# Performance work log

Measured on AMD Instinct MI355X. Metric: run time of the kernel, lower is better.

## Reference

```python
import jax, jax.numpy as jnp
import numpy as np

N = 50000          # nodes
E = 800000         # edges (avg degree 16)
T = 4              # edge types (edge_attr_dim)
H = 8              # heads
C1 = 16            # state_dim (per-head channels, layer 1)
C2 = 8             # out_dim  (per-head channels, layer 2)
D = 128            # node_attr_dim
NEG = -1e9         # masked-attention logit
LRELU_SLOPE = 0.2  # PyG GATConv default negative_slope


def setup_inputs() -> dict:
    key = jax.random.key(0)
    ks = jax.random.split(key, 12)
    x = jax.random.normal(ks[0], (N, D), jnp.float32)
    edge_src = jax.random.randint(ks[1], (E,), 0, N, jnp.int32)
    edge_dst = jax.random.randint(ks[2], (E,), 0, N, jnp.int32)
    edge_type = jax.random.randint(ks[3], (E,), 0, T, jnp.int32)
    W1 = jax.random.normal(ks[4], (T, D, H * C1), jnp.float32) * (1.0 / np.sqrt(D))
    a1_src = jax.random.normal(ks[5], (T, H, C1), jnp.float32) * 0.1
    a1_dst = jax.random.normal(ks[6], (T, H, C1), jnp.float32) * 0.1
    b1 = jnp.zeros((T, H * C1), jnp.float32)
    W2 = jax.random.normal(ks[7], (T, H * C1, H * C2), jnp.float32) * (1.0 / np.sqrt(H * C1))
    a2_src = jax.random.normal(ks[8], (T, H, C2), jnp.float32) * 0.1
    a2_dst = jax.random.normal(ks[9], (T, H, C2), jnp.float32) * 0.1
    b2 = jnp.zeros((T, H * C2), jnp.float32)
    return dict(x=x, edge_src=edge_src, edge_dst=edge_dst, edge_type=edge_type,
                W1=W1, a1_src=a1_src, a1_dst=a1_dst, b1=b1,
                W2=W2, a2_src=a2_src, a2_dst=a2_dst, b2=b2)


def gat_conv(x_in, W, a_src, a_dst, b, src, dst, mask, n):
    """One PyG-style GATConv (concat heads, eval mode) on masked edge list."""
    heads, c = a_src.shape
    h = (x_in @ W).reshape(n, heads, c)                       # [N,H,C]
    s_src = jnp.sum(h * a_src, axis=-1)                        # [N,H]
    s_dst = jnp.sum(h * a_dst, axis=-1)                        # [N,H]
    e = jax.nn.leaky_relu(s_src[src] + s_dst[dst], LRELU_SLOPE)  # [Et,H]
    e = jnp.where(mask[:, None], e, NEG)
    m = jax.ops.segment_max(e, dst, num_segments=n)            # [N,H]
    p = jnp.exp(e - m[dst]) * mask[:, None].astype(e.dtype)    # unnorm softmax
    denom = jax.ops.segment_sum(p, dst, num_segments=n)        # [N,H]
    msg = p[:, :, None] * h[src]                               # [Et,H,C]
    agg = jax.ops.segment_sum(msg, dst, num_segments=n)        # [N,H,C]
    out = agg / denom[:, :, None]
    return out.reshape(n, heads * c) + b


def reference(x, edge_src, edge_dst, edge_type, W1, a1_src, a1_dst, b1,
              W2, a2_src, a2_dst, b2):
    n = x.shape[0]
    loops = jnp.arange(n, dtype=edge_src.dtype)
    src = jnp.concatenate([edge_src, loops])   # self-loops appended (PyG default)
    dst = jnp.concatenate([edge_dst, loops])
    ones = jnp.ones((n,), bool)
    outs = []
    for t in range(T):
        mask = jnp.concatenate([edge_type == t, ones])
        h1 = gat_conv(x, W1[t], a1_src[t], a1_dst[t], b1[t], src, dst, mask, n)
        h1 = jax.nn.relu(h1)
        h2 = gat_conv(h1, W2[t], a2_src[t], a2_dst[t], b2[t], src, dst, mask, n)
        outs.append(h2)
    return jnp.concatenate(outs, axis=1)       # [N, T*H*C2]
```

## Files before the change

kernel.cpp:

```cpp
#include <hip/hip_runtime.h>
#include <cstddef>

constexpr int NN  = 50000;
constexpr int NE  = 800000;
constexpr int NT  = 4;
constexpr int NH  = 8;
constexpr int C1  = 16;
constexpr int C2  = 8;
constexpr int DD  = 128;
constexpr int HC1 = NH * C1;
constexpr int HC2 = NH * C2;
constexpr int CAP = 22;
constexpr int BSTRIDE = 48;
constexpr float SLOPE = 0.2f;

constexpr int G_ZERO = 2344;
constexpr int G_P1   = NT * 16384 / 256;
constexpr int G_P2   = NT * 8192 / 256;
constexpr int G_SCAT = 782;
constexpr int G_GEMM = NN / 16;
constexpr int G_GAT1 = NN / 16;
constexpr int G_GAT2 = (NN + 31) / 32;

using short8 = __attribute__((ext_vector_type(8))) short;
using f32x4  = __attribute__((ext_vector_type(4))) float;
typedef unsigned short u16;
typedef unsigned char  u8;

__device__ __forceinline__ float lrelu(float x) { return x > 0.f ? x : SLOPE * x; }
__device__ __forceinline__ float bfl(unsigned u) { return __uint_as_float(u << 16); }
__device__ __forceinline__ float bfh(unsigned u) { return __uint_as_float(u & 0xffff0000u); }
__device__ __forceinline__ u16 f2bf(float f) {
    unsigned u = __float_as_uint(f);
    return (u16)((u + 0x7fffu + ((u >> 16) & 1u)) >> 16);
}
__device__ __forceinline__ void deci8(uint2 v, float sc, float f[8]) {
    int w0 = (int)v.x, w1 = (int)v.y;
    f[0] = (float)((w0 << 24) >> 24) * sc;
    f[1] = (float)((w0 << 16) >> 24) * sc;
    f[2] = (float)((w0 <<  8) >> 24) * sc;
    f[3] = (float)( w0        >> 24) * sc;
    f[4] = (float)((w1 << 24) >> 24) * sc;
    f[5] = (float)((w1 << 16) >> 24) * sc;
    f[6] = (float)((w1 <<  8) >> 24) * sc;
    f[7] = (float)( w1        >> 24) * sc;
}
__device__ __forceinline__ float dotf(const float h[8], const float* a) {
    return h[0]*a[0] + h[1]*a[1] + h[2]*a[2] + h[3]*a[3]
         + h[4]*a[4] + h[5]*a[5] + h[6]*a[6] + h[7]*a[7];
}
__device__ __forceinline__ float dot8(uint4 hv, const float* a) {
    return bfl(hv.x) * a[0] + bfh(hv.x) * a[1] + bfl(hv.y) * a[2] + bfh(hv.y) * a[3]
         + bfl(hv.z) * a[4] + bfh(hv.z) * a[5] + bfl(hv.w) * a[6] + bfh(hv.w) * a[7];
}
__device__ __forceinline__ unsigned qperm(unsigned own, unsigned part, unsigned sel) {
    return __builtin_amdgcn_perm(own, part, sel);
}

__device__ __forceinline__ void scatter4(int e0, const int* __restrict__ esrc,
        const int* __restrict__ edst, const int* __restrict__ etyp,
        unsigned* __restrict__ bkt, int tmin, int tmax) {
    int bk[4], src[4];
    bool v[4];
    #pragma unroll
    for (int k = 0; k < 4; ++k) {
        int i = e0 + k * 256;
        bk[k] = 0; src[k] = 0;
        v[k] = false;
        if (i < NE) {
            int ty = etyp[i];
            v[k] = (ty >= tmin) && (ty <= tmax);
            if (v[k]) { bk[k] = ty * NN + edst[i]; src[k] = esrc[i]; }
        }
    }
    int slot[4];
    #pragma unroll
    for (int k = 0; k < 4; ++k)
        if (v[k]) slot[k] = atomicAdd((int*)((char*)bkt + (size_t)bk[k] * BSTRIDE), 1);
    #pragma unroll
    for (int k = 0; k < 4; ++k)
        if (v[k] && slot[k] < CAP)
            ((u16*)((char*)bkt + (size_t)bk[k] * BSTRIDE))[2 + slot[k]] = (u16)src[k];
}

__global__ __launch_bounds__(256) void init_kernel(const float* __restrict__ W1,
        u16* __restrict__ wp1, const float* __restrict__ W2, u16* __restrict__ wp2,
        unsigned* __restrict__ bkt) {
    const int b = blockIdx.x, tid = threadIdx.x;
    if (b < G_ZERO) {
        int i = b * 256 + tid;
        if (i < 600000) reinterpret_cast<uint4*>(bkt)[i] = make_uint4(0, 0, 0, 0);
    } else if (b < G_ZERO + G_P1) {
        int i = (b - G_ZERO) * 256 + tid;
        int t = i >> 14, r = i & 16383;
        int ntl = r >> 11, ks = (r >> 9) & 3, lane = (r >> 3) & 63, j = r & 7;
        int col = ntl * 16 + (lane & 15);
        int k   = ks * 32 + (lane >> 4) * 8 + j;
        wp1[i] = f2bf(W1[((size_t)t * DD + k) * HC1 + col]);
    } else {
        int i = (b - G_ZERO - G_P1) * 256 + tid;
        int t = i >> 13, r = i & 8191;
        int ntl = r >> 11, ks = (r >> 9) & 3, lane = (r >> 3) & 63, j = r & 7;
        int col = ntl * 16 + (lane & 15);
        int k   = ks * 32 + (lane >> 4) * 8 + j;
        wp2[i] = f2bf(W2[((size_t)t * HC1 + k) * HC2 + col]);
    }
}

__global__ __launch_bounds__(256) void scat_kernel(const int* __restrict__ esrc,
        const int* __restrict__ edst, const int* __restrict__ etyp,
        unsigned* __restrict__ bkt, int t) {
    scatter4(blockIdx.x * 1024 + threadIdx.x, esrc, edst, etyp, bkt, t, t);
}

__global__ __launch_bounds__(256) void gemm_kernel(const float* __restrict__ x,
        const u16* __restrict__ wp1, u8* __restrict__ h1, float* __restrict__ sc1) {
    constexpr int NTILE = HC1 / 16;
    __shared__ u16 xls[16][136];
    __shared__ unsigned st[4][16][36];
    const int bx = blockIdx.x, tid = threadIdx.x;
    const int w    = tid >> 6;
    const int lane = tid & 63;
    const int q    = lane >> 4;
    const int c    = lane & 15;
    const int rowbase = bx * 16;

    {
        int r = tid >> 4, g8 = tid & 15;
        const float4* xp = reinterpret_cast<const float4*>(
            x + (size_t)(rowbase + r) * DD + g8 * 8);
        float4 f0 = xp[0], f1 = xp[1];
        uint4 o;
        o.x = (unsigned)f2bf(f0.x) | ((unsigned)f2bf(f0.y) << 16);
        o.y = (unsigned)f2bf(f0.z) | ((unsigned)f2bf(f0.w) << 16);
        o.z = (unsigned)f2bf(f1.x) | ((unsigned)f2bf(f1.y) << 16);
        o.w = (unsigned)f2bf(f1.z) | ((unsigned)f2bf(f1.w) << 16);
        *reinterpret_cast<uint4*>(&xls[r][g8 * 8]) = o;
    }
    __syncthreads();

    short8 afrag[4];
    #pragma unroll
    for (int ks = 0; ks < 4; ++ks)
        afrag[ks] = *reinterpret_cast<const short8*>(&xls[c][q * 8 + ks * 32]);

    f32x4 acc[NTILE];
    #pragma unroll
    for (int ntl = 0; ntl < NTILE; ++ntl) acc[ntl] = (f32x4){0.f, 0.f, 0.f, 0.f};
    const short8* wp = reinterpret_cast<const short8*>(wp1 + (size_t)w * 16384) + lane;
    #pragma unroll
    for (int ntl = 0; ntl < NTILE; ++ntl)
        #pragma unroll
        for (int ks = 0; ks < 4; ++ks) {
            short8 b = wp[(ntl * 4 + ks) * 64];
            acc[ntl] = __builtin_amdgcn_mfma_f32_16x16x32_bf16(afrag[ks], b, acc[ntl], 0, 0, 0);
        }

    float mx[NTILE][4];
    #pragma unroll
    for (int ntl = 0; ntl < NTILE; ++ntl)
        #pragma unroll
        for (int reg = 0; reg < 4; ++reg) mx[ntl][reg] = fabsf(acc[ntl][reg]);
    #pragma unroll
    for (int m = 1; m < 16; m <<= 1)
        #pragma unroll
        for (int ntl = 0; ntl < NTILE; ++ntl)
            #pragma unroll
            for (int reg = 0; reg < 4; ++reg)
                mx[ntl][reg] = fmaxf(mx[ntl][reg], __shfl_xor(mx[ntl][reg], m));

    u8*    h1w = h1  + (size_t)w * NN * HC1;
    float* scw = sc1 + (size_t)w * NN * 8;

    #pragma unroll
    for (int reg = 0; reg < 4; ++reg) {
        unsigned w0 = 0, w1 = 0;
        #pragma unroll
        for (int ntl = 0; ntl < 4; ++ntl) {
            float m = mx[ntl][reg];
            float rs = m > 0.f ? 127.f / m : 0.f;
            int iv = __float2int_rn(acc[ntl][reg] * rs);
            w0 |= ((unsigned)iv & 0xffu) << (8 * ntl);
        }
        #pragma unroll
        for (int ntl = 4; ntl < 8; ++ntl) {
            float m = mx[ntl][reg];
            float rs = m > 0.f ? 127.f / m : 0.f;
            int iv = __float2int_rn(acc[ntl][reg] * rs);
            w1 |= ((unsigned)iv & 0xffu) << (8 * (ntl - 4));
        }
        unsigned sel1 = (c & 1) ? 0x07030501u : 0x02060004u;
        unsigned p0 = __shfl_xor(w0, 1), p1 = __shfl_xor(w1, 1);
        w0 = qperm(w0, p0, sel1);
        w1 = qperm(w1, p1, sel1);
        unsigned sel2 = (c & 2) ? 0x07060302u : 0x01000504u;
        p0 = __shfl_xor(w0, 2); p1 = __shfl_xor(w1, 2);
        w0 = qperm(w0, p0, sel2);
        w1 = qperm(w1, p1, sel2);
        st[w][q * 4 + reg][(c & 3) * 4 + (c >> 2)]      = w0;
        st[w][q * 4 + reg][(c & 3) * 4 + (c >> 2) + 16] = w1;
    }
    {
        int r0 = lane >> 3, dw = (lane & 7) * 4;
        uint4 v0 = *reinterpret_cast<const uint4*>(&st[w][r0][dw]);
        uint4 v1 = *reinterpret_cast<const uint4*>(&st[w][8 + r0][dw]);
        uint4* dst = reinterpret_cast<uint4*>(h1w + (size_t)rowbase * HC1);
        dst[lane]      = v0;
        dst[64 + lane] = v1;
    }
    {
        int reg = c >> 2, hp = c & 3;
        int row = rowbase + q * 4 + reg;
        float2 s;
        s.x = mx[2 * hp][reg] * (1.f / 127.f);
        s.y = mx[2 * hp + 1][reg] * (1.f / 127.f);
        reinterpret_cast<float2*>(scw)[(size_t)row * 4 + hp] = s;
    }
}

template<int TPN, bool SPLIT, bool I8>
__device__ __forceinline__ void gather_body(const unsigned* __restrict__ bkt, int bk,
        int q, const float* asr, float sdn, const void* __restrict__ hbase,
        const float* __restrict__ scp, float& den, float acc[8]) {
    const uint2* bp = reinterpret_cast<const uint2*>((const char*)bkt + (size_t)bk * BSTRIDE);
    unsigned w[12];
    #pragma unroll
    for (int i = 0; i < 6; ++i) { uint2 u = bp[i]; w[2 * i] = u.x; w[2 * i + 1] = u.y; }
    int deg = (int)w[0]; if (deg > CAP) deg = CAP;
    #pragma unroll
    for (int c = 0; c < 6; ++c) {
        if (c * 4 >= deg) break;
        unsigned lo = w[1 + 2 * c];
        unsigned hi = (c < 5) ? w[2 + 2 * c] : 0u;
        int sv[4] = {(int)(lo & 0xffff), (int)(lo >> 16),
                     (int)(hi & 0xffff), (int)(hi >> 16)};
        #pragma unroll
        for (int j = 0; j < 4; ++j) {
            if (c * 4 + j < deg) {
                int sn = sv[j];
                float hf[8];
                if constexpr (I8) {
                    uint2 hv = reinterpret_cast<const uint2*>(hbase)[(size_t)sn * TPN + q];
                    float sc = scp[(size_t)sn * 8 + (q >> 1)];
                    deci8(hv, sc, hf);
                } else {
                    uint4 hv = reinterpret_cast<const uint4*>(hbase)[(size_t)sn * TPN + q];
                    hf[0] = bfl(hv.x); hf[1] = bfh(hv.x);
                    hf[2] = bfl(hv.y); hf[3] = bfh(hv.y);
                    hf[4] = bfl(hv.z); hf[5] = bfh(hv.z);
                    hf[6] = bfl(hv.w); hf[7] = bfh(hv.w);
                }
                float d = dotf(hf, asr);
                if (SPLIT) d += __shfl_xor(d, 1);
                float pp = __expf(lrelu(d + sdn));
                den += pp;
                #pragma unroll
                for (int i = 0; i < 8; ++i) acc[i] += pp * hf[i];
            }
        }
    }
}

__global__ __launch_bounds__(256) void g1g2_kernel(const unsigned* __restrict__ bkt,
        int t, const u8* __restrict__ h1r, const float* __restrict__ sc1r,
        const float* __restrict__ a1s_t, const float* __restrict__ a1d_t,
        const float* __restrict__ b1t, const u16* __restrict__ wp2t,
        u16* __restrict__ h2w) {
    const int bx = blockIdx.x, tid = threadIdx.x;
    __shared__ u16 lt[16][136];
    const int node0 = bx * 16;
    const int nl    = tid >> 4;
    const int node  = node0 + nl;
    const int q     = tid & 15;
    const int head  = q >> 1;
    const int bk    = t * NN + node;

    float asr[8], adr[8];
    #pragma unroll
    for (int i = 0; i < 8; ++i) {
        asr[i] = a1s_t[head * C1 + (q & 1) * 8 + i];
        adr[i] = a1d_t[head * C1 + (q & 1) * 8 + i];
    }

    uint2 hv = reinterpret_cast<const uint2*>(h1r)[(size_t)node * 16 + q];
    float scn = sc1r[(size_t)node * 8 + head];
    float hs[8];
    deci8(hv, scn, hs);
    float ds = dotf(hs, asr); ds += __shfl_xor(ds, 1);
    float dd = dotf(hs, adr); dd += __shfl_xor(dd, 1);
    const float sdn = dd;

    float p = __expf(lrelu(ds + sdn));
    float den = p;
    float acc[8];
    #pragma unroll
    for (int i = 0; i < 8; ++i) acc[i] = p * hs[i];
    gather_body<16, true, true>(bkt, bk, q, asr, sdn, h1r, sc1r, den, acc);

    float inv = 1.f / den;
    uint4 ov;
    {
        float o[8];
        #pragma unroll
        for (int i = 0; i < 8; ++i)
            o[i] = fmaxf(acc[i] * inv + b1t[q * 8 + i], 0.f);
        ov.x = (unsigned)f2bf(o[0]) | ((unsigned)f2bf(o[1]) << 16);
        ov.y = (unsigned)f2bf(o[2]) | ((unsigned)f2bf(o[3]) << 16);
        ov.z = (unsigned)f2bf(o[4]) | ((unsigned)f2bf(o[5]) << 16);
        ov.w = (unsigned)f2bf(o[6]) | ((unsigned)f2bf(o[7]) << 16);
    }
    *reinterpret_cast<uint4*>(&lt[nl][q * 8]) = ov;
    __syncthreads();

    const int wave = tid >> 6;
    const int lane = tid & 63;
    const int quad = lane >> 4;
    const int c    = lane & 15;
    short8 af[4];
    #pragma unroll
    for (int ks = 0; ks < 4; ++ks)
        af[ks] = *reinterpret_cast<const short8*>(&lt[c][ks * 32 + quad * 8]);
    f32x4 cacc = (f32x4){0.f, 0.f, 0.f, 0.f};
    const short8* wp = reinterpret_cast<const short8*>(wp2t) + lane;
    #pragma unroll
    for (int ks = 0; ks < 4; ++ks)
        cacc = __builtin_amdgcn_mfma_f32_16x16x32_bf16(af[ks], wp[(wave * 4 + ks) * 64], cacc, 0, 0, 0);

    const int col = wave * 16 + c;
    #pragma unroll
    for (int reg = 0; reg < 4; ++reg) {
        int row = node0 + quad * 4 + reg;
        h2w[(size_t)row * HC2 + col] = f2bf(cacc[reg]);
    }
}

__global__ __launch_bounds__(256) void gat2_kernel(const unsigned* __restrict__ bkt,
        int t, const u16* __restrict__ h2r, const float* __restrict__ a2s_t,
        const float* __restrict__ a2d_t, const float* __restrict__ b2t,
        float* __restrict__ out) {
    const int bx = blockIdx.x, tid = threadIdx.x;
    const int node = bx * 32 + (tid >> 3);
    if (node >= NN) return;
    const int q    = tid & 7;
    const int head = q;
    const int bk   = t * NN + node;
    const uint4* __restrict__ h4 = reinterpret_cast<const uint4*>(h2r);

    float asr[8], adr[8];
    #pragma unroll
    for (int i = 0; i < 8; ++i) {
        asr[i] = a2s_t[head * C2 + i];
        adr[i] = a2d_t[head * C2 + i];
    }

    uint4 hv = h4[(size_t)node * 8 + q];
    const float sdn = dot8(hv, adr);
    float p = __expf(lrelu(dot8(hv, asr) + sdn));
    float den = p;
    float acc[8];
    acc[0] = p * bfl(hv.x); acc[1] = p * bfh(hv.x);
    acc[2] = p * bfl(hv.y); acc[3] = p * bfh(hv.y);
    acc[4] = p * bfl(hv.z); acc[5] = p * bfh(hv.z);
    acc[6] = p * bfl(hv.w); acc[7] = p * bfh(hv.w);
    gather_body<8, false, false>(bkt, bk, q, asr, sdn, h2r, nullptr, den, acc);

    float inv = 1.f / den;
    float o[8];
    #pragma unroll
    for (int i = 0; i < 8; ++i) o[i] = acc[i] * inv + b2t[q * 8 + i];
    float* op = out + (size_t)node * (NT * HC2) + t * HC2 + q * 8;
    reinterpret_cast<float4*>(op)[0] = make_float4(o[0], o[1], o[2], o[3]);
    reinterpret_cast<float4*>(op)[1] = make_float4(o[4], o[5], o[6], o[7]);
}

extern "C" void kernel_launch(void* const* d_in, const int* in_sizes, int n_in,
                              void* d_out, int out_size, void* d_ws, size_t ws_size,
                              hipStream_t stream) {
    const float* x    = (const float*)d_in[0];
    const int*   esrc = (const int*)d_in[1];
    const int*   edst = (const int*)d_in[2];
    const int*   etyp = (const int*)d_in[3];
    const float* W1   = (const float*)d_in[4];
    const float* a1s  = (const float*)d_in[5];
    const float* a1d  = (const float*)d_in[6];
    const float* b1   = (const float*)d_in[7];
    const float* W2   = (const float*)d_in[8];
    const float* a2s  = (const float*)d_in[9];
    const float* a2d  = (const float*)d_in[10];
    const float* b2   = (const float*)d_in[11];
    float* out = (float*)d_out;
    char* base = (char*)d_ws;

    u8*    h1  = (u8*)base;
    float* sc1 = (float*)(base + 25600000);
    u16*   h2d[2] = {(u16*)(base + 32000000), (u16*)(base + 38400000)};
    unsigned* bkt = (unsigned*)(base + 44800000);
    u16* wp1 = (u16*)(base + 54400000);
    u16* wp2 = (u16*)(base + 54531072);

    dim3 blk(256);
    hipLaunchKernelGGL(init_kernel, dim3(G_ZERO + G_P1 + G_P2), blk, 0, stream,
                       W1, wp1, W2, wp2, bkt);
    for (int t = 0; t < 4; ++t)
        hipLaunchKernelGGL(scat_kernel, dim3(G_SCAT), blk, 0, stream,
                           esrc, edst, etyp, bkt, t);
    hipLaunchKernelGGL(gemm_kernel, dim3(G_GEMM), blk, 0, stream,
                       x, wp1, h1, sc1);

    auto g1g2 = [&](int t) {
        hipLaunchKernelGGL(g1g2_kernel, dim3(G_GAT1), blk, 0, stream,
                           bkt, t, h1 + (size_t)t * NN * HC1, sc1 + (size_t)t * NN * 8,
                           a1s + t * NH * C1, a1d + t * NH * C1, b1 + t * HC1,
                           wp2 + (size_t)t * 8192, h2d[t & 1]);
    };
    auto gat2 = [&](int t) {
        hipLaunchKernelGGL(gat2_kernel, dim3(G_GAT2), blk, 0, stream,
                           bkt, t, h2d[t & 1], a2s + t * NH * C2, a2d + t * NH * C2,
                           b2 + t * HC2, out);
    };
    g1g2(0); g1g2(1); gat2(0); g1g2(2); gat2(1); g1g2(3); gat2(2); gat2(3);
}
```

Baseline: 323.7 us.

## Split neighbor gather across two sub-groups and fuse scatter with layer-1 GEMM

The four per-type scatter launches become a single pass that buckets all edges by their own type, and that pass is fused with the layer-1 GEMM into one launch with block-range dispatch. Both GAT gather kernels now assign two thread groups per node, each handling alternate neighbors, and combine partial sums with a shuffle. This doubles the threads available for latency-bound gathers. The costs are idle threads in the MFMA stage and output writes, extra shuffles, and a 512-thread block size for g1g2 that may limit occupancy.

New measurement: 321.2 us. Within noise of the previous version (-0.8%).

```diff
diff --git a/kernel.cpp b/kernel.cpp
--- a/kernel.cpp
+++ b/kernel.cpp
@@ -20,7 +20,7 @@
 constexpr int G_SCAT = 782;
 constexpr int G_GEMM = NN / 16;
 constexpr int G_GAT1 = NN / 16;
-constexpr int G_GAT2 = (NN + 31) / 32;
+constexpr int G_GAT2 = NN / 16;
 
 using short8 = __attribute__((ext_vector_type(8))) short;
 using f32x4  = __attribute__((ext_vector_type(4))) float;
@@ -59,19 +59,15 @@
 
 __device__ __forceinline__ void scatter4(int e0, const int* __restrict__ esrc,
         const int* __restrict__ edst, const int* __restrict__ etyp,
-        unsigned* __restrict__ bkt, int tmin, int tmax) {
+        unsigned* __restrict__ bkt) {
     int bk[4], src[4];
     bool v[4];
     #pragma unroll
     for (int k = 0; k < 4; ++k) {
         int i = e0 + k * 256;
+        v[k] = i < NE;
         bk[k] = 0; src[k] = 0;
-        v[k] = false;
-        if (i < NE) {
-            int ty = etyp[i];
-            v[k] = (ty >= tmin) && (ty <= tmax);
-            if (v[k]) { bk[k] = ty * NN + edst[i]; src[k] = esrc[i]; }
-        }
+        if (v[k]) { bk[k] = etyp[i] * NN + edst[i]; src[k] = esrc[i]; }
     }
     int slot[4];
     #pragma unroll
@@ -107,18 +103,11 @@
     }
 }
 
-__global__ __launch_bounds__(256) void scat_kernel(const int* __restrict__ esrc,
-        const int* __restrict__ edst, const int* __restrict__ etyp,
-        unsigned* __restrict__ bkt, int t) {
-    scatter4(blockIdx.x * 1024 + threadIdx.x, esrc, edst, etyp, bkt, t, t);
-}
-
-__global__ __launch_bounds__(256) void gemm_kernel(const float* __restrict__ x,
+__device__ __forceinline__ void gemm_body(int bx, int tid, const float* __restrict__ x,
         const u16* __restrict__ wp1, u8* __restrict__ h1, float* __restrict__ sc1) {
     constexpr int NTILE = HC1 / 16;
     __shared__ u16 xls[16][136];
     __shared__ unsigned st[4][16][36];
-    const int bx = blockIdx.x, tid = threadIdx.x;
     const int w    = tid >> 6;
     const int lane = tid & 63;
     const int q    = lane >> 4;
@@ -218,9 +207,19 @@
     }
 }
 
+__global__ __launch_bounds__(256) void scatgemm_kernel(
+        const int* __restrict__ esrc, const int* __restrict__ edst,
+        const int* __restrict__ etyp, unsigned* __restrict__ bkt,
+        const float* __restrict__ x, const u16* __restrict__ wp1,
+        u8* __restrict__ h1, float* __restrict__ sc1) {
+    const int b = blockIdx.x, tid = threadIdx.x;
+    if (b < G_SCAT) scatter4(b * 1024 + tid, esrc, edst, etyp, bkt);
+    else gemm_body(b - G_SCAT, tid, x, wp1, h1, sc1);
+}
+
 template<int TPN, bool SPLIT, bool I8>
 __device__ __forceinline__ void gather_body(const unsigned* __restrict__ bkt, int bk,
-        int q, const float* asr, float sdn, const void* __restrict__ hbase,
+        int sub, int q, const float* asr, float sdn, const void* __restrict__ hbase,
         const float* __restrict__ scp, float& den, float acc[8]) {
     const uint2* bp = reinterpret_cast<const uint2*>((const char*)bkt + (size_t)bk * BSTRIDE);
     unsigned w[12];
@@ -235,7 +234,8 @@
         int sv[4] = {(int)(lo & 0xffff), (int)(lo >> 16),
                      (int)(hi & 0xffff), (int)(hi >> 16)};
         #pragma unroll
-        for (int j = 0; j < 4; ++j) {
+        for (int jj = 0; jj < 2; ++jj) {
+            int j = sub + 2 * jj;
             if (c * 4 + j < deg) {
                 int sn = sv[j];
                 float hf[8];
@@ -261,7 +261,7 @@
     }
 }
 
-__global__ __launch_bounds__(256) void g1g2_kernel(const unsigned* __restrict__ bkt,
+__global__ __launch_bounds__(512) void g1g2_kernel(const unsigned* __restrict__ bkt,
         int t, const u8* __restrict__ h1r, const float* __restrict__ sc1r,
         const float* __restrict__ a1s_t, const float* __restrict__ a1d_t,
         const float* __restrict__ b1t, const u16* __restrict__ wp2t,
@@ -269,8 +269,9 @@
     const int bx = blockIdx.x, tid = threadIdx.x;
     __shared__ u16 lt[16][136];
     const int node0 = bx * 16;
-    const int nl    = tid >> 4;
+    const int nl    = tid >> 5;
     const int node  = node0 + nl;
+    const int sub   = (tid >> 4) & 1;
     const int q     = tid & 15;
     const int head  = q >> 1;
     const int bk    = t * NN + node;
@@ -290,47 +291,59 @@
     float dd = dotf(hs, adr); dd += __shfl_xor(dd, 1);
     const float sdn = dd;
 
-    float p = __expf(lrelu(ds + sdn));
-    float den = p;
-    float acc[8];
-    #pragma unroll
-    for (int i = 0; i < 8; ++i) acc[i] = p * hs[i];
-    gather_body<16, true, true>(bkt, bk, q, asr, sdn, h1r, sc1r, den, acc);
+    float den, acc[8];
+    if (sub == 0) {
+        float p = __expf(lrelu(ds + sdn));
+        den = p;
+        #pragma unroll
+        for (int i = 0; i < 8; ++i) acc[i] = p * hs[i];
+    } else {
+        den = 0.f;
+        #pragma unroll
+        for (int i = 0; i < 8; ++i) acc[i] = 0.f;
+    }
+    gather_body<16, true, true>(bkt, bk, sub, q, asr, sdn, h1r, sc1r, den, acc);
+
+    den += __shfl_xor(den, 16);
+    #pragma unroll
+    for (int i = 0; i < 8; ++i) acc[i] += __shfl_xor(acc[i], 16);
 
     float inv = 1.f / den;
-    uint4 ov;
-    {
+    if (sub == 0) {
         float o[8];
         #pragma unroll
         for (int i = 0; i < 8; ++i)
             o[i] = fmaxf(acc[i] * inv + b1t[q * 8 + i], 0.f);
+        uint4 ov;
         ov.x = (unsigned)f2bf(o[0]) | ((unsigned)f2bf(o[1]) << 16);
         ov.y = (unsigned)f2bf(o[2]) | ((unsigned)f2bf(o[3]) << 16);
         ov.z = (unsigned)f2bf(o[4]) | ((unsigned)f2bf(o[5]) << 16);
         ov.w = (unsigned)f2bf(o[6]) | ((unsigned)f2bf(o[7]) << 16);
-    }
-    *reinterpret_cast<uint4*>(&lt[nl][q * 8]) = ov;
+        *reinterpret_cast<uint4*>(&lt[nl][q * 8]) = ov;
+    }
     __syncthreads();
 
-    const int wave = tid >> 6;
-    const int lane = tid & 63;
-    const int quad = lane >> 4;
-    const int c    = lane & 15;
-    short8 af[4];
-    #pragma unroll
-    for (int ks = 0; ks < 4; ++ks)
-        af[ks] = *reinterpret_cast<const short8*>(&lt[c][ks * 32 + quad * 8]);
-    f32x4 cacc = (f32x4){0.f, 0.f, 0.f, 0.f};
-    const short8* wp = reinterpret_cast<const short8*>(wp2t) + lane;
-    #pragma unroll
-    for (int ks = 0; ks < 4; ++ks)
-        cacc = __builtin_amdgcn_mfma_f32_16x16x32_bf16(af[ks], wp[(wave * 4 + ks) * 64], cacc, 0, 0, 0);
-
-    const int col = wave * 16 + c;
-    #pragma unroll
-    for (int reg = 0; reg < 4; ++reg) {
-        int row = node0 + quad * 4 + reg;
-        h2w[(size_t)row * HC2 + col] = f2bf(cacc[reg]);
+    if (tid < 256) {
+        const int wave = tid >> 6;
+        const int lane = tid & 63;
+        const int quad = lane >> 4;
+        const int c    = lane & 15;
+        short8 af[4];
+        #pragma unroll
+        for (int ks = 0; ks < 4; ++ks)
+            af[ks] = *reinterpret_cast<const short8*>(&lt[c][ks * 32 + quad * 8]);
+        f32x4 cacc = (f32x4){0.f, 0.f, 0.f, 0.f};
+        const short8* wp = reinterpret_cast<const short8*>(wp2t) + lane;
+        #pragma unroll
+        for (int ks = 0; ks < 4; ++ks)
+            cacc = __builtin_amdgcn_mfma_f32_16x16x32_bf16(af[ks], wp[(wave * 4 + ks) * 64], cacc, 0, 0, 0);
+
+        const int col = wave * 16 + c;
+        #pragma unroll
+        for (int reg = 0; reg < 4; ++reg) {
+            int row = node0 + quad * 4 + reg;
+            h2w[(size_t)row * HC2 + col] = f2bf(cacc[reg]);
+        }
     }
 }
 
@@ -339,8 +352,9 @@
         const float* __restrict__ a2d_t, const float* __restrict__ b2t,
         float* __restrict__ out) {
     const int bx = blockIdx.x, tid = threadIdx.x;
-    const int node = bx * 32 + (tid >> 3);
+    const int node = bx * 16 + (tid >> 4);
     if (node >= NN) return;
+    const int sub  = (tid >> 3) & 1;
     const int q    = tid & 7;
     const int head = q;
     const int bk   = t * NN + node;
@@ -355,22 +369,34 @@
 
     uint4 hv = h4[(size_t)node * 8 + q];
     const float sdn = dot8(hv, adr);
-    float p = __expf(lrelu(dot8(hv, asr) + sdn));
-    float den = p;
-    float acc[8];
-    acc[0] = p * bfl(hv.x); acc[1] = p * bfh(hv.x);
-    acc[2] = p * bfl(hv.y); acc[3] = p * bfh(hv.y);
-    acc[4] = p * bfl(hv.z); acc[5] = p * bfh(hv.z);
-    acc[6] = p * bfl(hv.w); acc[7] = p * bfh(hv.w);
-    gather_body<8, false, false>(bkt, bk, q, asr, sdn, h2r, nullptr, den, acc);
-
-    float inv = 1.f / den;
-    float o[8];
-    #pragma unroll
-    for (int i = 0; i < 8; ++i) o[i] = acc[i] * inv + b2t[q * 8 + i];
-    float* op = out + (size_t)node * (NT * HC2) + t * HC2 + q * 8;
-    reinterpret_cast<float4*>(op)[0] = make_float4(o[0], o[1], o[2], o[3]);
-    reinterpret_cast<float4*>(op)[1] = make_float4(o[4], o[5], o[6], o[7]);
+    float den, acc[8];
+    if (sub == 0) {
+        float p = __expf(lrelu(dot8(hv, asr) + sdn));
+        den = p;
+        acc[0] = p * bfl(hv.x); acc[1] = p * bfh(hv.x);
+        acc[2] = p * bfl(hv.y); acc[3] = p * bfh(hv.y);
+        acc[4] = p * bfl(hv.z); acc[5] = p * bfh(hv.z);
+        acc[6] = p * bfl(hv.w); acc[7] = p * bfh(hv.w);
+    } else {
+        den = 0.f;
+        #pragma unroll
+        for (int i = 0; i < 8; ++i) acc[i] = 0.f;
+    }
+    gather_body<8, false, false>(bkt, bk, sub, q, asr, sdn, h2r, nullptr, den, acc);
+
+    den += __shfl_xor(den, 8);
+    #pragma unroll
+    for (int i = 0; i < 8; ++i) acc[i] += __shfl_xor(acc[i], 8);
+
+    if (sub == 0) {
+        float inv = 1.f / den;
+        float o[8];
+        #pragma unroll
+        for (int i = 0; i < 8; ++i) o[i] = acc[i] * inv + b2t[q * 8 + i];
+        float* op = out + (size_t)node * (NT * HC2) + t * HC2 + q * 8;
+        reinterpret_cast<float4*>(op)[0] = make_float4(o[0], o[1], o[2], o[3]);
+        reinterpret_cast<float4*>(op)[1] = make_float4(o[4], o[5], o[6], o[7]);
+    }
 }
 
 extern "C" void kernel_launch(void* const* d_in, const int* in_sizes, int n_in,
@@ -398,23 +424,19 @@
     u16* wp1 = (u16*)(base + 54400000);
     u16* wp2 = (u16*)(base + 54531072);
 
-    dim3 blk(256);
-    hipLaunchKernelGGL(init_kernel, dim3(G_ZERO + G_P1 + G_P2), blk, 0, stream,
+    hipLaunchKernelGGL(init_kernel, dim3(G_ZERO + G_P1 + G_P2), dim3(256), 0, stream,
                        W1, wp1, W2, wp2, bkt);
-    for (int t = 0; t < 4; ++t)
-        hipLaunchKernelGGL(scat_kernel, dim3(G_SCAT), blk, 0, stream,
-                           esrc, edst, etyp, bkt, t);
-    hipLaunchKernelGGL(gemm_kernel, dim3(G_GEMM), blk, 0, stream,
-                       x, wp1, h1, sc1);
+    hipLaunchKernelGGL(scatgemm_kernel, dim3(G_SCAT + G_GEMM), dim3(256), 0, stream,
+                       esrc, edst, etyp, bkt, x, wp1, h1, sc1);
 
     auto g1g2 = [&](int t) {
-        hipLaunchKernelGGL(g1g2_kernel, dim3(G_GAT1), blk, 0, stream,
+        hipLaunchKernelGGL(g1g2_kernel, dim3(G_GAT1), dim3(512), 0, stream,
                            bkt, t, h1 + (size_t)t * NN * HC1, sc1 + (size_t)t * NN * 8,
                            a1s + t * NH * C1, a1d + t * NH * C1, b1 + t * HC1,
                            wp2 + (size_t)t * 8192, h2d[t & 1]);
     };
     auto gat2 = [&](int t) {
-        hipLaunchKernelGGL(gat2_kernel, dim3(G_GAT2), blk, 0, stream,
+        hipLaunchKernelGGL(gat2_kernel, dim3(G_GAT2), dim3(256), 0, stream,
                            bkt, t, h2d[t & 1], a2s + t * NH * C2, a2d + t * NH * C2,
                            b2 + t * HC2, out);
     };
```
